# Kernel optimization log

Hardware: AMD Instinct MI355X
Metric: run time of the kernel (lower is better)

Reference implementation:

```python
import jax, jax.numpy as jnp
import numpy as np

DIM, HEADS, DIM_HEAD = 1024, 16, 64
DIM_INNER = HEADS * DIM_HEAD  # 1024
SCALE = DIM_HEAD ** -0.5


def _rope(t):
    # t: [b, h, n, d]; interleaved-pair RoPE (lucidrains rotary-embedding-torch default)
    d = t.shape[-1]
    n = t.shape[-2]
    inv_freq = 1.0 / (10000.0 ** (jnp.arange(0, d, 2, dtype=jnp.float32) / d))
    angles = jnp.arange(n, dtype=jnp.float32)[:, None] * inv_freq[None, :]  # [n, d/2]
    cos, sin = jnp.cos(angles), jnp.sin(angles)
    t1, t2 = t[..., 0::2], t[..., 1::2]
    r1 = t1 * cos - t2 * sin
    r2 = t1 * sin + t2 * cos
    return jnp.stack([r1, r2], axis=-1).reshape(t.shape)


def setup_inputs() -> dict:
    key = jax.random.key(0)
    ks = jax.random.split(key, 8)
    b, n = 2, 2048
    inp = {
        "x": jax.random.normal(ks[0], (b, n, DIM), dtype=jnp.float32),
        "value_residual": jax.random.normal(ks[1], (b, HEADS, n, DIM_HEAD), dtype=jnp.float32),
        "gamma": jnp.ones((DIM,), dtype=jnp.float32),
        "w_qkv": jax.random.normal(ks[2], (DIM, 3 * DIM_INNER), dtype=jnp.float32) * (DIM ** -0.5),
        "w_mix": jax.random.normal(ks[3], (DIM, HEADS), dtype=jnp.float32) * (DIM ** -0.5),
        "b_mix": jnp.zeros((HEADS,), dtype=jnp.float32),
        "w_gates": jax.random.normal(ks[4], (DIM, HEADS), dtype=jnp.float32) * (DIM ** -0.5),
        "b_gates": jnp.zeros((HEADS,), dtype=jnp.float32),
        "w_out": jax.random.normal(ks[5], (DIM_INNER, DIM), dtype=jnp.float32) * (DIM_INNER ** -0.5),
    }
    return inp


def reference(x, value_residual, gamma, w_qkv, w_mix, b_mix, w_gates, b_gates, w_out):
    b, n, _ = x.shape
    # RMSNorm (lucidrains style: F.normalize * sqrt(dim) * gamma)
    norm = jnp.sqrt(jnp.sum(x * x, axis=-1, keepdims=True))
    xn = x / jnp.maximum(norm, 1e-12) * (DIM ** 0.5) * gamma

    qkv = xn @ w_qkv  # [b, n, 3*h*d]
    qkv = qkv.reshape(b, n, 3, HEADS, DIM_HEAD)
    q, k, v = [jnp.transpose(qkv[:, :, i], (0, 2, 1, 3)) for i in range(3)]  # [b,h,n,d]
    original_values = v

    # learned value-residual lerp
    mix = jax.nn.sigmoid(xn @ w_mix + b_mix)            # [b, n, h]
    mix = jnp.transpose(mix, (0, 2, 1))[..., None]       # [b, h, n, 1]
    v = v * (1.0 - mix) + value_residual * mix

    # rotary on q, k
    q = _rope(q)
    k = _rope(k)

    scores = jnp.einsum("bhid,bhjd->bhij", q, k) * SCALE
    attn = jax.nn.softmax(scores, axis=-1)
    out = jnp.einsum("bhij,bhjd->bhid", attn, v)         # [b, h, n, d]

    gates = jax.nn.sigmoid(xn @ w_gates + b_gates)       # [b, n, h]
    out = out * jnp.transpose(gates, (0, 2, 1))[..., None]

    out = jnp.transpose(out, (0, 2, 1, 3)).reshape(b, n, DIM_INNER)
    return out @ w_out, original_values
```

## Files before the change

kernel.cpp:

```cpp
#include <hip/hip_runtime.h>
#include <hip/hip_bf16.h>
#include <math.h>

#define DIMSZ 1024
#define HEADS 16
#define DHEAD 64
#define NSEQ  2048
#define BATCH 2
#define ROWS  (BATCH*NSEQ)
#define SCALE 0.125f
#define LOG2E 1.4426950408889634f

typedef __attribute__((ext_vector_type(8))) short short8;
typedef __attribute__((ext_vector_type(4))) float floatx4;

#define MFMA16(a,b,c) __builtin_amdgcn_mfma_f32_16x16x32_bf16(a,b,c,0,0,0)

__device__ __forceinline__ void gl2lds16(const void* g, void* l) {
    __builtin_amdgcn_global_load_lds(
        (const __attribute__((address_space(1))) unsigned int*)g,
        (__attribute__((address_space(3))) unsigned int*)l, 16, 0, 0);
}

__device__ __forceinline__ unsigned short bf16r(float a) {
    unsigned u = __float_as_uint(a);
    u += 0x7fff + ((u >> 16) & 1);
    return (unsigned short)(u >> 16);
}
__device__ __forceinline__ unsigned pack_bf16(float a, float b) {
    unsigned ua = __float_as_uint(a), ub = __float_as_uint(b);
    ua += 0x7fff + ((ua >> 16) & 1);
    ub += 0x7fff + ((ub >> 16) & 1);
    return (ua >> 16) | (ub & 0xffff0000u);
}
__device__ __forceinline__ float2 bf2f(unsigned u) {
    float2 r;
    r.x = __uint_as_float(u << 16);
    r.y = __uint_as_float(u & 0xffff0000u);
    return r;
}
__device__ __forceinline__ float fexp2(float x) {
#if __has_builtin(__builtin_amdgcn_exp2f)
    return __builtin_amdgcn_exp2f(x);
#else
    return exp2f(x);
#endif
}
__device__ __forceinline__ float fsin_rev(float x) {
#if __has_builtin(__builtin_amdgcn_sinf)
    return __builtin_amdgcn_sinf(x);
#else
    return __sinf(x * 6.28318530717958647692f);
#endif
}
__device__ __forceinline__ float fcos_rev(float x) {
#if __has_builtin(__builtin_amdgcn_cosf)
    return __builtin_amdgcn_cosf(x);
#else
    return __cosf(x * 6.28318530717958647692f);
#endif
}

__global__ __launch_bounds__(256) void transpose_all_kernel(
    const float* __restrict__ w_qkv, const float* __restrict__ w_out,
    const float* __restrict__ w_mix, const float* __restrict__ w_gates,
    unsigned short* __restrict__ wqkvT, unsigned short* __restrict__ woutT,
    unsigned short* __restrict__ wmgT)
{
    __shared__ float t[32][33];
    const int tx = threadIdx.x & 31, tyy = threadIdx.x >> 5;
    const int bx = blockIdx.x;
    const int k0 = blockIdx.y * 32;
    if (bx < 128) {
        const float* src;
        unsigned short* dst;
        int N, n0;
        if (bx < 96) { src = w_qkv; dst = wqkvT; N = 3*DIMSZ; n0 = bx*32; }
        else         { src = w_out; dst = woutT; N = DIMSZ;   n0 = (bx-96)*32; }
        #pragma unroll
        for (int i = 0; i < 4; i++)
            t[tyy*4 + i][tx] = src[(size_t)(k0 + tyy*4 + i)*N + n0 + tx];
        __syncthreads();
        #pragma unroll
        for (int i = 0; i < 4; i++)
            dst[(size_t)(n0 + tyy*4 + i)*DIMSZ + k0 + tx] = bf16r(t[tx][tyy*4 + i]);
    } else {
        #pragma unroll
        for (int i = 0; i < 4; i++) {
            const int kk = k0 + tyy*4 + i;
            t[tyy*4 + i][tx] = (tx < 16) ? w_mix[kk*16 + tx]
                                         : w_gates[kk*16 + (tx - 16)];
        }
        __syncthreads();
        #pragma unroll
        for (int i = 0; i < 4; i++)
            wmgT[(size_t)(tyy*4 + i)*DIMSZ + k0 + tx] = bf16r(t[tx][tyy*4 + i]);
    }
}

__global__ __launch_bounds__(256) void rmsnorm_kernel(
    const float* __restrict__ x, const float* __restrict__ gamma,
    unsigned short* __restrict__ xnb)
{
    const int row = blockIdx.x;
    const int tid = threadIdx.x;
    __shared__ float wred[4];

    const float4 xv = ((const float4*)(x + (size_t)row * DIMSZ))[tid];
    float ss = xv.x*xv.x + xv.y*xv.y + xv.z*xv.z + xv.w*xv.w;
    #pragma unroll
    for (int off = 1; off < 64; off <<= 1) ss += __shfl_xor(ss, off);
    if ((tid & 63) == 0) wred[tid >> 6] = ss;
    __syncthreads();
    const float total = wred[0] + wred[1] + wred[2] + wred[3];
    const float inv = 32.0f / fmaxf(sqrtf(total), 1e-12f);
    const float4 gv = ((const float4*)gamma)[tid];
    uint2 pk;
    pk.x = pack_bf16(xv.x * inv * gv.x, xv.y * inv * gv.y);
    pk.y = pack_bf16(xv.z * inv * gv.z, xv.w * inv * gv.w);
    ((uint2*)(xnb + (size_t)row * DIMSZ))[tid] = pk;
}

__global__ __launch_bounds__(256) void mix_gates_mfma(
    const unsigned short* __restrict__ A, const unsigned short* __restrict__ WG,
    const float* __restrict__ b_mix, const float* __restrict__ b_gates,
    float* __restrict__ mixo, float* __restrict__ gateso)
{
    __shared__ short As[128*32];
    __shared__ short Bs[32*32];
    const int tid = threadIdx.x;
    const int wv = tid >> 6, lane = tid & 63;
    const int g = lane >> 4, c = lane & 15;
    const int bm = blockIdx.x * 128;

    floatx4 acc[2][2];
    #pragma unroll
    for (int mt = 0; mt < 2; mt++)
        #pragma unroll
        for (int nt = 0; nt < 2; nt++) acc[mt][nt] = (floatx4){0.f,0.f,0.f,0.f};

    for (int k0 = 0; k0 < DIMSZ; k0 += 32) {
        __syncthreads();
        #pragma unroll
        for (int r = 0; r < 2; r++) {
            const int ch = tid + 256*r;
            const int row = ch >> 2, cc = ch & 3;
            gl2lds16(A + (size_t)(bm + row)*DIMSZ + k0 + cc*8, (void*)(As + ch*8));
        }
        if (tid < 128)
            gl2lds16(WG + (size_t)(tid >> 2)*DIMSZ + k0 + (tid & 3)*8, (void*)(Bs + tid*8));
        __syncthreads();
        short8 af[2], bf[2];
        #pragma unroll
        for (int mt = 0; mt < 2; mt++) af[mt] = *(const short8*)(As + (wv*32 + mt*16 + c)*32 + g*8);
        #pragma unroll
        for (int nt = 0; nt < 2; nt++) bf[nt] = *(const short8*)(Bs + (nt*16 + c)*32 + g*8);
        #pragma unroll
        for (int mt = 0; mt < 2; mt++)
            #pragma unroll
            for (int nt = 0; nt < 2; nt++)
                acc[mt][nt] = MFMA16(af[mt], bf[nt], acc[mt][nt]);
    }
    const float bm_c = b_mix[c], bg_c = b_gates[c];
    #pragma unroll
    for (int mt = 0; mt < 2; mt++)
        #pragma unroll
        for (int r2 = 0; r2 < 4; r2++) {
            const int row = bm + wv*32 + mt*16 + g*4 + r2;
            const float lm = acc[mt][0][r2] + bm_c;
            const float lg = acc[mt][1][r2] + bg_c;
            mixo[(size_t)row*HEADS + c]   = 1.0f / (1.0f + fexp2(-lm * LOG2E));
            gateso[(size_t)row*HEADS + c] = 1.0f / (1.0f + fexp2(-lg * LOG2E));
        }
}

__global__ __launch_bounds__(256) void gemm_qkv_mfma(
    const unsigned short* __restrict__ A, const unsigned short* __restrict__ BT,
    unsigned short* __restrict__ qb, unsigned short* __restrict__ kb,
    float* __restrict__ vb)
{
    __shared__ short As[128*32];
    __shared__ short Bs[128*32];
    const int tid = threadIdx.x;
    const int wv = tid >> 6, lane = tid & 63;
    const int g = lane >> 4, c = lane & 15;
    const int wm = wv >> 1, wn = wv & 1;
    const int bm = blockIdx.y * 128, bn = blockIdx.x * 128;

    floatx4 acc[4][4];
    #pragma unroll
    for (int mt = 0; mt < 4; mt++)
        #pragma unroll
        for (int nt = 0; nt < 4; nt++) acc[mt][nt] = (floatx4){0.f,0.f,0.f,0.f};

    for (int k0 = 0; k0 < DIMSZ; k0 += 32) {
        __syncthreads();
        #pragma unroll
        for (int r = 0; r < 2; r++) {
            const int ch = tid + 256*r;
            const int row = ch >> 2, cc = ch & 3;
            gl2lds16(A  + (size_t)(bm + row)*DIMSZ + k0 + cc*8, (void*)(As + ch*8));
            gl2lds16(BT + (size_t)(bn + row)*DIMSZ + k0 + cc*8, (void*)(Bs + ch*8));
        }
        __syncthreads();
        short8 af[4], bf[4];
        #pragma unroll
        for (int mt = 0; mt < 4; mt++) af[mt] = *(const short8*)(As + (wm*64 + mt*16 + c)*32 + g*8);
        #pragma unroll
        for (int nt = 0; nt < 4; nt++) bf[nt] = *(const short8*)(Bs + (wn*64 + nt*16 + c)*32 + g*8);
        #pragma unroll
        for (int mt = 0; mt < 4; mt++)
            #pragma unroll
            for (int nt = 0; nt < 4; nt++)
                acc[mt][nt] = MFMA16(af[mt], bf[nt], acc[mt][nt]);
    }
    __syncthreads();
    const int i3 = bn >> 10;
    const int nb = bn - (i3 << 10);
    if (i3 < 2) {
        unsigned short* dst = (i3 == 0) ? qb : kb;
        short* wbuf = As + wv*1152;
        const int rd_row = lane >> 2, seg = lane & 3;
        #pragma unroll
        for (int mt = 0; mt < 4; mt++) {
            #pragma unroll
            for (int nt = 0; nt < 4; nt++)
                #pragma unroll
                for (int r2 = 0; r2 < 4; r2++)
                    wbuf[(g*4 + r2)*72 + nt*16 + c] = (short)bf16r(acc[mt][nt][r2]);
            __builtin_amdgcn_s_waitcnt(0xc07f);
            const uint4 v0 = *(const uint4*)&wbuf[rd_row*72 + seg*16];
            const uint4 v1 = *(const uint4*)&wbuf[rd_row*72 + seg*16 + 8];
            const int row = bm + wm*64 + mt*16 + rd_row;
            const int col = nb + wn*64 + seg*16;
            const int hh = col >> 6, dd = col & 63;
            const int bb2 = row >> 11, pos = row & 2047;
            unsigned short* dp = dst + (((size_t)(bb2*HEADS + hh)*NSEQ) + pos)*DHEAD + dd;
            *(uint4*)dp = v0;
            *(uint4*)(dp + 8) = v1;
            __builtin_amdgcn_s_waitcnt(0xc07f);
        }
    } else {
        #pragma unroll
        for (int mt = 0; mt < 4; mt++)
            #pragma unroll
            for (int nt = 0; nt < 4; nt++)
                #pragma unroll
                for (int r2 = 0; r2 < 4; r2++) {
                    const int row = bm + wm*64 + mt*16 + g*4 + r2;
                    const int col = nb + wn*64 + nt*16 + c;
                    const int hh = col >> 6, dd = col & 63;
                    const int bb2 = row >> 11, pos = row & 2047;
                    vb[(((size_t)(bb2*HEADS + hh)*NSEQ) + pos)*DHEAD + dd] = acc[mt][nt][r2];
                }
    }
}

__global__ __launch_bounds__(256) void rope_blend_kernel2(
    unsigned short* __restrict__ q, unsigned short* __restrict__ k,
    const float* __restrict__ vorig, const float* __restrict__ vres,
    const float* __restrict__ mixb, unsigned short* __restrict__ vT)
{
    __shared__ unsigned short vt[64*72];
    const int tid = threadIdx.x;
    const int bh = blockIdx.y, bb = bh >> 4, h = bh & 15;
    const int p0 = blockIdx.x * 64;
    {
        const int pr = tid >> 2, d0 = (tid & 3) * 16;
        const int pos = p0 + pr;
        const size_t base = ((size_t)bh*NSEQ + pos)*DHEAD + d0;

        uint4 qr0 = *(uint4*)(q + base), qr1 = *(uint4*)(q + base + 8);
        uint4 kr0 = *(uint4*)(k + base), kr1 = *(uint4*)(k + base + 8);
        unsigned qw[8] = {qr0.x, qr0.y, qr0.z, qr0.w, qr1.x, qr1.y, qr1.z, qr1.w};
        unsigned kw[8] = {kr0.x, kr0.y, kr0.z, kr0.w, kr1.x, kr1.y, kr1.z, kr1.w};
        const float QSC = SCALE * LOG2E;
        const float posf = (float)pos;
        #pragma unroll
        for (int j = 0; j < 8; j++) {
            const float pf = (float)((d0 >> 1) + j);
            const float rev = posf * fexp2(-pf * 0.41524101186092029f
                                           - 2.6514961294723187f);
            const float rf = rev - floorf(rev);
            const float sn = fsin_rev(rf);
            const float cs = fcos_rev(rf);
            float2 qv = bf2f(qw[j]);
            float2 kv = bf2f(kw[j]);
            const float q1 = qv.x*cs - qv.y*sn, q2 = qv.x*sn + qv.y*cs;
            const float k1 = kv.x*cs - kv.y*sn, k2 = kv.x*sn + kv.y*cs;
            qw[j] = pack_bf16(q1*QSC, q2*QSC);
            kw[j] = pack_bf16(k1, k2);
        }
        *(uint4*)(q + base)     = *(uint4*)(qw + 0);
        *(uint4*)(q + base + 8) = *(uint4*)(qw + 4);
        *(uint4*)(k + base)     = *(uint4*)(kw + 0);
        *(uint4*)(k + base + 8) = *(uint4*)(kw + 4);

        float vv[16], vr[16];
        #pragma unroll
        for (int i = 0; i < 4; i++) {
            *(float4*)(vv + i*4) = *(const float4*)(vorig + base + i*4);
            *(float4*)(vr + i*4) = *(const float4*)(vres + base + i*4);
        }
        const float mx = mixb[((size_t)(bb*NSEQ + pos))*HEADS + h];
        #pragma unroll
        for (int j = 0; j < 8; j++) {
            const float b0 = vv[2*j]*(1.f-mx)   + vr[2*j]*mx;
            const float b1 = vv[2*j+1]*(1.f-mx) + vr[2*j+1]*mx;
            vt[pr*72 + d0 + 2*j]     = bf16r(b0);
            vt[pr*72 + d0 + 2*j + 1] = bf16r(b1);
        }
    }
    __syncthreads();
    {
        const int dd = tid >> 2, c0 = (tid & 3) * 16;
        unsigned o[8];
        #pragma unroll
        for (int j = 0; j < 8; j++) {
            const unsigned a  = vt[(c0 + 2*j)*72 + dd];
            const unsigned b2 = vt[(c0 + 2*j + 1)*72 + dd];
            o[j] = a | (b2 << 16);
        }
        unsigned short* dst = vT + ((size_t)bh*DHEAD + dd)*NSEQ + p0 + c0;
        *(uint4*)(dst)     = *(uint4*)(o + 0);
        *(uint4*)(dst + 8) = *(uint4*)(o + 4);
    }
}

__global__ __launch_bounds__(512) void attn_mfma_kernel(
    const unsigned short* __restrict__ qg,
    const unsigned short* __restrict__ kg,
    const unsigned short* __restrict__ vT,
    const float* __restrict__ gates,
    unsigned short* __restrict__ outp)
{
    __shared__ short KV[16384];
    __shared__ short Ps[16384];

    short* Kt = KV;
    short* Vt = KV + 8192;

    const int tid = threadIdx.x;
    const int w = tid >> 6, lane = tid & 63;
    const int wq = w & 3, s = w >> 2;
    const int g = lane >> 4, c = lane & 15;
    const int bh = blockIdx.y, bb = bh >> 4, h = bh & 15;
    const int q0 = blockIdx.x * 128;

    short8 qf[2][2];
    #pragma unroll
    for (int mt = 0; mt < 2; mt++)
        #pragma unroll
        for (int kb = 0; kb < 2; kb++)
            qf[mt][kb] = *(const short8*)(qg + ((size_t)bh*NSEQ + q0 + wq*32 + mt*16 + c)*DHEAD + kb*32 + g*8);

    floatx4 O[2][4];
    #pragma unroll
    for (int mt = 0; mt < 2; mt++)
        #pragma unroll
        for (int nt = 0; nt < 4; nt++) O[mt][nt] = (floatx4){0.f,0.f,0.f,0.f};
    float lsum[2] = {0.f, 0.f};

    short* PsW = Ps + w * 2048;
    short* Kts = Kt + s * 4096;
    short* Vts = Vt + s * 4096;
    const unsigned short* kbase = kg + (size_t)bh*NSEQ*DHEAD;
    const unsigned short* vbase = vT + (size_t)bh*DHEAD*NSEQ;

    for (int kt2 = 0; kt2 < 16; kt2++) {
        __syncthreads();
        #pragma unroll
        for (int r = 0; r < 2; r++) {
            const int ch = tid + 512*r;
            const int t  = ch >> 9;
            const int cw = ch & 511;
            const int row = cw >> 3;
            const int u = (cw & 7) ^ (row & 7);
            const int ktile = kt2 + 16*t;
            gl2lds16(kbase + (size_t)(ktile*64 + row)*DHEAD + u*8, (void*)(Kt + t*4096 + cw*8));
            gl2lds16(vbase + (size_t)row*NSEQ + ktile*64 + u*8,   (void*)(Vt + t*4096 + cw*8));
        }
        __syncthreads();

        short8 kfr[4][2];
        #pragma unroll
        for (int nt = 0; nt < 4; nt++) {
            const int rowk = nt*16 + c;
            #pragma unroll
            for (int kb = 0; kb < 2; kb++)
                kfr[nt][kb] = *(const short8*)(Kts + rowk*64 + (((kb*4 + g) ^ (rowk & 7)) * 8));
        }

        #pragma unroll
        for (int mt = 0; mt < 2; mt++) {
            const int rr = mt*16 + c;
            #pragma unroll
            for (int nt = 0; nt < 4; nt++) {
                floatx4 accS = (floatx4){0.f,0.f,0.f,0.f};
                #pragma unroll
                for (int kb = 0; kb < 2; kb++)
                    accS = MFMA16(kfr[nt][kb], qf[mt][kb], accS);
                const float p0 = fexp2(accS[0]);
                const float p1 = fexp2(accS[1]);
                const float p2 = fexp2(accS[2]);
                const float p3 = fexp2(accS[3]);
                lsum[mt] += (p0 + p1) + (p2 + p3);
                uint2 pk;
                pk.x = pack_bf16(p0, p1);
                pk.y = pack_bf16(p2, p3);
                *(uint2*)(PsW + rr*64 + (((nt*2 + (g >> 1)) ^ (rr & 7)) * 8) + (g & 1)*4) = pk;
            }
        }
        __builtin_amdgcn_s_waitcnt(0xc07f);
        #pragma unroll
        for (int kb = 0; kb < 2; kb++) {
            short8 pf[2];
            #pragma unroll
            for (int mt = 0; mt < 2; mt++) {
                const int rr = mt*16 + c;
                pf[mt] = *(const short8*)(PsW + rr*64 + (((kb*4 + g) ^ (rr & 7)) * 8));
            }
            #pragma unroll
            for (int nt = 0; nt < 4; nt++) {
                const int rv = nt*16 + c;
                short8 vf = *(const short8*)(Vts + rv*64 + (((kb*4 + g) ^ (rv & 7)) * 8));
                #pragma unroll
                for (int mt = 0; mt < 2; mt++)
                    O[mt][nt] = MFMA16(pf[mt], vf, O[mt][nt]);
            }
        }
    }

    __syncthreads();
    float* cb = (float*)KV;
    float* lf = (float*)Ps;
    if (s == 1) {
        #pragma unroll
        for (int mt = 0; mt < 2; mt++) {
            #pragma unroll
            for (int nt = 0; nt < 4; nt++)
                #pragma unroll
                for (int r2 = 0; r2 < 4; r2++)
                    cb[wq*2048 + ((mt*4 + nt)*4 + r2)*64 + lane] = O[mt][nt][r2];
            lf[wq*128 + mt*64 + lane] = lsum[mt];
        }
    }
    __syncthreads();
    if (s == 0) {
        #pragma unroll
        for (int mt = 0; mt < 2; mt++) {
            #pragma unroll
            for (int nt = 0; nt < 4; nt++)
                #pragma unroll
                for (int r2 = 0; r2 < 4; r2++)
                    O[mt][nt][r2] += cb[wq*2048 + ((mt*4 + nt)*4 + r2)*64 + lane];
            lsum[mt] += lf[wq*128 + mt*64 + lane];
        }
        #pragma unroll
        for (int mt = 0; mt < 2; mt++) {
            float l = lsum[mt];
            l += __shfl_xor(l, 16);
            l += __shfl_xor(l, 32);
            #pragma unroll
            for (int r2 = 0; r2 < 4; r2++) {
                const float lr = __shfl(l, g*4 + r2);
                const int rowg = q0 + wq*32 + mt*16 + g*4 + r2;
                const float gt = gates[((size_t)(bb*NSEQ + rowg))*HEADS + h];
                const float sc = gt / lr;
                unsigned short* op = outp + ((size_t)(bb*NSEQ + rowg))*DIMSZ + h*DHEAD + c;
                #pragma unroll
                for (int nt = 0; nt < 4; nt++)
                    op[nt*16] = bf16r(O[mt][nt][r2] * sc);
            }
        }
    }
}

__global__ __launch_bounds__(256) void gemm_out_mfma(
    const unsigned short* __restrict__ A, const unsigned short* __restrict__ BT,
    float* __restrict__ out0)
{
    __shared__ short As[128*32];
    __shared__ short Bs[128*32];
    const int tid = threadIdx.x;
    const int wv = tid >> 6, lane = tid & 63;
    const int g = lane >> 4, c = lane & 15;
    const int wm = wv >> 1, wn = wv & 1;
    const int bm = blockIdx.y * 128, bn = blockIdx.x * 128;

    floatx4 acc[4][4];
    #pragma unroll
    for (int mt = 0; mt < 4; mt++)
        #pragma unroll
        for (int nt = 0; nt < 4; nt++) acc[mt][nt] = (floatx4){0.f,0.f,0.f,0.f};

    for (int k0 = 0; k0 < DIMSZ; k0 += 32) {
        __syncthreads();
        #pragma unroll
        for (int r = 0; r < 2; r++) {
            const int ch = tid + 256*r;
            const int row = ch >> 2, cc = ch & 3;
            gl2lds16(A  + (size_t)(bm + row)*DIMSZ + k0 + cc*8, (void*)(As + ch*8));
            gl2lds16(BT + (size_t)(bn + row)*DIMSZ + k0 + cc*8, (void*)(Bs + ch*8));
        }
        __syncthreads();
        short8 af[4], bf[4];
        #pragma unroll
        for (int mt = 0; mt < 4; mt++) af[mt] = *(const short8*)(As + (wm*64 + mt*16 + c)*32 + g*8);
        #pragma unroll
        for (int nt = 0; nt < 4; nt++) bf[nt] = *(const short8*)(Bs + (wn*64 + nt*16 + c)*32 + g*8);
        #pragma unroll
        for (int mt = 0; mt < 4; mt++)
            #pragma unroll
            for (int nt = 0; nt < 4; nt++)
                acc[mt][nt] = MFMA16(af[mt], bf[nt], acc[mt][nt]);
    }
    #pragma unroll
    for (int mt = 0; mt < 4; mt++)
        #pragma unroll
        for (int nt = 0; nt < 4; nt++)
            #pragma unroll
            for (int r2 = 0; r2 < 4; r2++) {
                const int row = bm + wm*64 + mt*16 + g*4 + r2;
                const int col = bn + wn*64 + nt*16 + c;
                out0[(size_t)row*DIMSZ + col] = acc[mt][nt][r2];
            }
}

extern "C" void kernel_launch(void* const* d_in, const int* in_sizes, int n_in,
                              void* d_out, int out_size, void* d_ws, size_t ws_size,
                              hipStream_t stream) {
    const float* x       = (const float*)d_in[0];
    const float* vres    = (const float*)d_in[1];
    const float* gamma   = (const float*)d_in[2];
    const float* w_qkv   = (const float*)d_in[3];
    const float* w_mix   = (const float*)d_in[4];
    const float* b_mix   = (const float*)d_in[5];
    const float* w_gates = (const float*)d_in[6];
    const float* b_gates = (const float*)d_in[7];
    const float* w_out   = (const float*)d_in[8];

    float* out0 = (float*)d_out;
    float* out1 = out0 + (size_t)ROWS * DIMSZ;

    char* ws = (char*)d_ws;
    unsigned short* xnb   = (unsigned short*)(ws);
    unsigned short* wqkvT = (unsigned short*)(ws + (8u<<20));
    unsigned short* woutT = (unsigned short*)(ws + (14u<<20));
    unsigned short* qb2   = (unsigned short*)(ws + (16u<<20));
    unsigned short* kb2   = (unsigned short*)(ws + (24u<<20));
    unsigned short* vT    = (unsigned short*)(ws + (32u<<20));
    unsigned short* attnO = (unsigned short*)(ws + (40u<<20));
    float*          mixb  = (float*)(ws + (48u<<20));
    float*          gatesb= (float*)(ws + (48u<<20) + 262144);
    unsigned short* wmgT  = (unsigned short*)(ws + (49u<<20));

    transpose_all_kernel<<<dim3(129, DIMSZ/32), 256, 0, stream>>>(
        w_qkv, w_out, w_mix, w_gates, wqkvT, woutT, wmgT);

    rmsnorm_kernel<<<ROWS, 256, 0, stream>>>(x, gamma, xnb);

    mix_gates_mfma<<<ROWS/128, 256, 0, stream>>>(
        xnb, wmgT, b_mix, b_gates, mixb, gatesb);

    gemm_qkv_mfma<<<dim3(3*DIMSZ/128, ROWS/128), 256, 0, stream>>>(
        xnb, wqkvT, qb2, kb2, out1);

    rope_blend_kernel2<<<dim3(NSEQ/64, BATCH*HEADS), 256, 0, stream>>>(
        qb2, kb2, out1, vres, mixb, vT);

    attn_mfma_kernel<<<dim3(NSEQ/128, BATCH*HEADS), 512, 0, stream>>>(
        qb2, kb2, vT, gatesb, attnO);

    gemm_out_mfma<<<dim3(DIMSZ/128, ROWS/128), 256, 0, stream>>>(
        attnO, woutT, out0);
}
```

Measured before the change: 276.2 us.

## Split attention KV range across separate blocks and add a combine kernel

The two KV halves were previously handled by two wave groups inside one 512-thread block and merged through LDS. They now run in separate 256-thread blocks, which doubles the grid and shrinks LDS per block. Each block writes bf16 partial outputs and row sums to global memory, and a new combine kernel adds the halves and applies the normalization and gate. This raises occupancy and block count at the cost of extra global traffic, an extra launch, and a loss of precision because the partials are rounded to bf16 before they are summed.

```diff
diff --git a/kernel.cpp b/kernel.cpp
--- a/kernel.cpp
+++ b/kernel.cpp
@@ -327,24 +327,24 @@
     }
 }
 
-__global__ __launch_bounds__(512) void attn_mfma_kernel(
+__global__ __launch_bounds__(256) void attn_mfma_kernel(
     const unsigned short* __restrict__ qg,
     const unsigned short* __restrict__ kg,
     const unsigned short* __restrict__ vT,
-    const float* __restrict__ gates,
-    unsigned short* __restrict__ outp)
-{
-    __shared__ short KV[16384];
-    __shared__ short Ps[16384];
-
-    short* Kt = KV;
-    short* Vt = KV + 8192;
+    unsigned short* __restrict__ Op0,
+    unsigned short* __restrict__ Op1,
+    float* __restrict__ lpart)
+{
+    __shared__ short Kt[64*64];
+    __shared__ short Vt[64*64];
+    __shared__ short Ps[4*32*64];
 
     const int tid = threadIdx.x;
     const int w = tid >> 6, lane = tid & 63;
-    const int wq = w & 3, s = w >> 2;
     const int g = lane >> 4, c = lane & 15;
-    const int bh = blockIdx.y, bb = bh >> 4, h = bh & 15;
+    const int byy = blockIdx.y;
+    const int bh = byy >> 1, s = byy & 1;
+    const int bb = bh >> 4, h = bh & 15;
     const int q0 = blockIdx.x * 128;
 
     short8 qf[2][2];
@@ -352,7 +352,7 @@
     for (int mt = 0; mt < 2; mt++)
         #pragma unroll
         for (int kb = 0; kb < 2; kb++)
-            qf[mt][kb] = *(const short8*)(qg + ((size_t)bh*NSEQ + q0 + wq*32 + mt*16 + c)*DHEAD + kb*32 + g*8);
+            qf[mt][kb] = *(const short8*)(qg + ((size_t)bh*NSEQ + q0 + w*32 + mt*16 + c)*DHEAD + kb*32 + g*8);
 
     floatx4 O[2][4];
     #pragma unroll
@@ -362,23 +362,19 @@
     float lsum[2] = {0.f, 0.f};
 
     short* PsW = Ps + w * 2048;
-    short* Kts = Kt + s * 4096;
-    short* Vts = Vt + s * 4096;
     const unsigned short* kbase = kg + (size_t)bh*NSEQ*DHEAD;
     const unsigned short* vbase = vT + (size_t)bh*DHEAD*NSEQ;
 
-    for (int kt2 = 0; kt2 < 16; kt2++) {
+    for (int i = 0; i < 16; i++) {
+        const int kt = s*16 + i;
         __syncthreads();
         #pragma unroll
         for (int r = 0; r < 2; r++) {
-            const int ch = tid + 512*r;
-            const int t  = ch >> 9;
-            const int cw = ch & 511;
-            const int row = cw >> 3;
-            const int u = (cw & 7) ^ (row & 7);
-            const int ktile = kt2 + 16*t;
-            gl2lds16(kbase + (size_t)(ktile*64 + row)*DHEAD + u*8, (void*)(Kt + t*4096 + cw*8));
-            gl2lds16(vbase + (size_t)row*NSEQ + ktile*64 + u*8,   (void*)(Vt + t*4096 + cw*8));
+            const int ch = tid + 256*r;
+            const int row = ch >> 3;
+            const int u = (ch & 7) ^ (row & 7);
+            gl2lds16(kbase + (size_t)(kt*64 + row)*DHEAD + u*8, (void*)(Kt + ch*8));
+            gl2lds16(vbase + (size_t)row*NSEQ + kt*64 + u*8,   (void*)(Vt + ch*8));
         }
         __syncthreads();
 
@@ -388,7 +384,7 @@
             const int rowk = nt*16 + c;
             #pragma unroll
             for (int kb = 0; kb < 2; kb++)
-                kfr[nt][kb] = *(const short8*)(Kts + rowk*64 + (((kb*4 + g) ^ (rowk & 7)) * 8));
+                kfr[nt][kb] = *(const short8*)(Kt + rowk*64 + (((kb*4 + g) ^ (rowk & 7)) * 8));
         }
 
         #pragma unroll
@@ -423,7 +419,7 @@
             #pragma unroll
             for (int nt = 0; nt < 4; nt++) {
                 const int rv = nt*16 + c;
-                short8 vf = *(const short8*)(Vts + rv*64 + (((kb*4 + g) ^ (rv & 7)) * 8));
+                short8 vf = *(const short8*)(Vt + rv*64 + (((kb*4 + g) ^ (rv & 7)) * 8));
                 #pragma unroll
                 for (int mt = 0; mt < 2; mt++)
                     O[mt][nt] = MFMA16(pf[mt], vf, O[mt][nt]);
@@ -431,49 +427,52 @@
         }
     }
 
-    __syncthreads();
-    float* cb = (float*)KV;
-    float* lf = (float*)Ps;
-    if (s == 1) {
-        #pragma unroll
-        for (int mt = 0; mt < 2; mt++) {
+    unsigned short* Op = s ? Op1 : Op0;
+    #pragma unroll
+    for (int mt = 0; mt < 2; mt++) {
+        float l = lsum[mt];
+        l += __shfl_xor(l, 16);
+        l += __shfl_xor(l, 32);
+        if (g == 0) {
+            const int rowl = q0 + w*32 + mt*16 + c;
+            lpart[((size_t)s*ROWS + bb*NSEQ + rowl)*HEADS + h] = l;
+        }
+        #pragma unroll
+        for (int r2 = 0; r2 < 4; r2++) {
+            const int rowg = q0 + w*32 + mt*16 + g*4 + r2;
+            unsigned short* op = Op + ((size_t)(bb*NSEQ + rowg))*DIMSZ + h*DHEAD + c;
             #pragma unroll
             for (int nt = 0; nt < 4; nt++)
-                #pragma unroll
-                for (int r2 = 0; r2 < 4; r2++)
-                    cb[wq*2048 + ((mt*4 + nt)*4 + r2)*64 + lane] = O[mt][nt][r2];
-            lf[wq*128 + mt*64 + lane] = lsum[mt];
-        }
-    }
-    __syncthreads();
-    if (s == 0) {
-        #pragma unroll
-        for (int mt = 0; mt < 2; mt++) {
-            #pragma unroll
-            for (int nt = 0; nt < 4; nt++)
-                #pragma unroll
-                for (int r2 = 0; r2 < 4; r2++)
-                    O[mt][nt][r2] += cb[wq*2048 + ((mt*4 + nt)*4 + r2)*64 + lane];
-            lsum[mt] += lf[wq*128 + mt*64 + lane];
-        }
-        #pragma unroll
-        for (int mt = 0; mt < 2; mt++) {
-            float l = lsum[mt];
-            l += __shfl_xor(l, 16);
-            l += __shfl_xor(l, 32);
-            #pragma unroll
-            for (int r2 = 0; r2 < 4; r2++) {
-                const float lr = __shfl(l, g*4 + r2);
-                const int rowg = q0 + wq*32 + mt*16 + g*4 + r2;
-                const float gt = gates[((size_t)(bb*NSEQ + rowg))*HEADS + h];
-                const float sc = gt / lr;
-                unsigned short* op = outp + ((size_t)(bb*NSEQ + rowg))*DIMSZ + h*DHEAD + c;
-                #pragma unroll
-                for (int nt = 0; nt < 4; nt++)
-                    op[nt*16] = bf16r(O[mt][nt][r2] * sc);
-            }
-        }
-    }
+                op[nt*16] = bf16r(O[mt][nt][r2]);
+        }
+    }
+}
+
+__global__ __launch_bounds__(256) void attn_combine_kernel(
+    const unsigned short* __restrict__ Op1, const float* __restrict__ lpart,
+    const float* __restrict__ gates, unsigned short* __restrict__ attnO)
+{
+    const int idx = blockIdx.x * 256 + threadIdx.x;
+    const int row = idx >> 7;
+    const int c8 = (idx & 127) * 8;
+    const int h = c8 >> 6;
+    const float l0 = lpart[(size_t)row*HEADS + h];
+    const float l1 = lpart[((size_t)ROWS + row)*HEADS + h];
+    const float gt = gates[(size_t)row*HEADS + h];
+    const float sc = gt / (l0 + l1);
+    const size_t base = (size_t)row*DIMSZ + c8;
+    const uint4 a = *(const uint4*)(attnO + base);
+    const uint4 b = *(const uint4*)(Op1 + base);
+    const unsigned aw[4] = {a.x, a.y, a.z, a.w};
+    const unsigned bw[4] = {b.x, b.y, b.z, b.w};
+    unsigned o[4];
+    #pragma unroll
+    for (int j = 0; j < 4; j++) {
+        const float2 fa = bf2f(aw[j]);
+        const float2 fb = bf2f(bw[j]);
+        o[j] = pack_bf16((fa.x + fb.x)*sc, (fa.y + fb.y)*sc);
+    }
+    *(uint4*)(attnO + base) = *(uint4*)o;
 }
 
 __global__ __launch_bounds__(256) void gemm_out_mfma(
@@ -554,6 +553,8 @@
     float*          mixb  = (float*)(ws + (48u<<20));
     float*          gatesb= (float*)(ws + (48u<<20) + 262144);
     unsigned short* wmgT  = (unsigned short*)(ws + (49u<<20));
+    unsigned short* Op1   = (unsigned short*)(ws + (50u<<20));
+    float*          lpart = (float*)(ws + (58u<<20));
 
     transpose_all_kernel<<<dim3(129, DIMSZ/32), 256, 0, stream>>>(
         w_qkv, w_out, w_mix, w_gates, wqkvT, woutT, wmgT);
@@ -569,8 +570,11 @@
     rope_blend_kernel2<<<dim3(NSEQ/64, BATCH*HEADS), 256, 0, stream>>>(
         qb2, kb2, out1, vres, mixb, vT);
 
-    attn_mfma_kernel<<<dim3(NSEQ/128, BATCH*HEADS), 512, 0, stream>>>(
-        qb2, kb2, vT, gatesb, attnO);
+    attn_mfma_kernel<<<dim3(NSEQ/128, BATCH*HEADS*2), 256, 0, stream>>>(
+        qb2, kb2, vT, attnO, Op1, lpart);
+
+    attn_combine_kernel<<<ROWS*DIMSZ/8/256, 256, 0, stream>>>(
+        Op1, lpart, gatesb, attnO);
 
     gemm_out_mfma<<<dim3(DIMSZ/128, ROWS/128), 256, 0, stream>>>(
         attnO, woutT, out0);
```

New measurement: 259.7 us. -6.0%, faster.
